# Kernel tuning notes

Measured on AMD Instinct MI355X. Metric: run time of the kernel, lower is better.

## Reference

```python
import jax, jax.numpy as jnp
import numpy as np

N, F, E, G = 50000, 128, 1600000, 64
CH = [16, 32, 64, 128, 256]
K = 3
EPS = 1e-5


def setup_inputs() -> dict:
    key = jax.random.key(0)
    ks = jax.random.split(key, 16)
    inp = {}
    inp["x"] = jax.random.normal(ks[0], (N, F), jnp.float32)
    inp["edge_weight"] = jax.random.uniform(ks[1], (E,), jnp.float32)
    inp["edge_index"] = jax.random.randint(ks[2], (2, E), 0, N)
    inp["batch_index"] = jnp.sort(jax.random.randint(ks[3], (N,), 0, G))
    dims = [F] + CH
    i = 4
    for l in range(5):
        fi, fo = dims[l], dims[l + 1]
        inp[f"W{l+1}"] = jax.random.normal(ks[i], (K, fi, fo), jnp.float32) / np.sqrt(K * fi)
        i += 1
        inp[f"b{l+1}"] = jnp.zeros((fo,), jnp.float32)
        if l < 4:  # no BN after the 5th conv
            inp[f"g{l+1}"] = jnp.ones((fo,), jnp.float32)
            inp[f"be{l+1}"] = jnp.zeros((fo,), jnp.float32)
    inp["Wd"] = jax.random.normal(ks[i], (2 * CH[-1], 4), jnp.float32) / np.sqrt(2 * CH[-1])
    inp["bd"] = jnp.zeros((4,), jnp.float32)
    inp["num_graphs"] = G
    return inp


def _bn(h, g, b):
    m = jnp.mean(h, axis=0)
    v = jnp.mean(jnp.square(h - m), axis=0)  # biased variance (torch training mode)
    return g * (h - m) / jnp.sqrt(v + EPS) + b


def reference(x, edge_weight, W1, b1, g1, be1, W2, b2, g2, be2, W3, b3, g3, be3,
              W4, b4, g4, be4, W5, b5, Wd, bd, edge_index, batch_index, num_graphs):
    n = x.shape[0]
    row, col = edge_index[0], edge_index[1]
    # sym-normalized Laplacian, lambda_max=2 -> scaled L_hat has zero diagonal,
    # off-diagonal = -w * deg^-1/2[row] * deg^-1/2[col]
    deg = jax.ops.segment_sum(edge_weight, row, num_segments=n)
    dinv = jnp.where(deg > 0, jax.lax.rsqrt(jnp.where(deg > 0, deg, 1.0)), 0.0)
    norm = -edge_weight * dinv[row] * dinv[col]

    def prop(z):  # L_hat @ z via sparse gather/scatter over edges
        return jax.ops.segment_sum(norm[:, None] * z[col], row, num_segments=n)

    def cheb(z, W, b):  # T0=z, T1=L z, T2=2 L T1 - T0
        t1 = prop(z)
        out = z @ W[0] + t1 @ W[1]
        t2 = 2.0 * prop(t1) - z
        return out + t2 @ W[2] + b

    h = _bn(jax.nn.softplus(cheb(x, W1, b1)), g1, be1)
    h = _bn(jax.nn.softplus(cheb(h, W2, b2)), g2, be2)
    h = _bn(jax.nn.softplus(cheb(h, W3, b3)), g3, be3)
    h = _bn(jax.nn.softplus(cheb(h, W4, b4)), g4, be4)
    h = cheb(h, W5, b5)

    mx = jax.ops.segment_max(h, batch_index, num_segments=num_graphs)
    mx = jnp.where(jnp.isfinite(mx), mx, 0.0)  # guard empty segments
    cnt = jax.ops.segment_sum(jnp.ones((n,), h.dtype), batch_index, num_segments=num_graphs)
    mean = jax.ops.segment_sum(h, batch_index, num_segments=num_graphs) / jnp.maximum(cnt, 1.0)[:, None]
    pooled = jnp.concatenate([mx, mean], axis=1)  # [G, 512]
    logits = pooled @ Wd + bd
    return jax.nn.log_softmax(logits, axis=-1)
```

## Files before the change

### kernel.cpp

```cpp
#include <hip/hip_runtime.h>
#include <hip/hip_fp16.h>
#include <cmath>

#define NN 50000
#define NE 1600000
#define NG 64
#define CAP 96
#define NPART 8
#define PROWS 6250

typedef __attribute__((ext_vector_type(8))) short short8_t;
typedef __attribute__((ext_vector_type(4))) float floatx4;
typedef __attribute__((ext_vector_type(4))) unsigned short us4;
typedef __attribute__((ext_vector_type(8))) unsigned short us8;

static __device__ __forceinline__ float softplusf(float x) {
    return fmaxf(x, 0.0f) + log1pf(expf(-fabsf(x)));
}

static __device__ __forceinline__ float bf2f(unsigned short u) {
    return __uint_as_float(((unsigned)u) << 16);
}
static __device__ __forceinline__ unsigned short f2bf(float x) {
    unsigned u = __float_as_uint(x);
    unsigned t = (u >> 16) & 1u;
    return (unsigned short)((u + 0x7FFFu + t) >> 16);
}
static __device__ __forceinline__ float h2f(unsigned u) {
    __half_raw r; r.x = (unsigned short)(u & 0xFFFFu);
    return __half2float(__half(r));
}
static __device__ __forceinline__ unsigned short f2h(float x) {
    __half h = __float2half_rn(x);
    return static_cast<__half_raw>(h).x;
}

static __device__ __forceinline__ void split_bf16(float x, unsigned short& hi, unsigned short& lo) {
    unsigned u = __float_as_uint(x);
    unsigned hb = u & 0xFFFF0000u;
    hi = (unsigned short)(hb >> 16);
    float r = x - __uint_as_float(hb);
    lo = f2bf(r);
}

__global__ __launch_bounds__(256) void k_slot2(const int* __restrict__ row,
                                               const int* __restrict__ col,
                                               const float* __restrict__ w,
                                               int* __restrict__ cnt,
                                               unsigned* __restrict__ pslots) {
    const int part = blockIdx.x & (NPART - 1);
    const int bid = blockIdx.x >> 3;
    const int nb = gridDim.x >> 3;
    const int rlo = part * PROWS;
    const int rhi = rlo + PROWS;
    for (int e = bid * 256 + threadIdx.x; e < NE; e += nb * 256) {
        int r = row[e];
        if (r >= rlo && r < rhi) {
            int k = atomicAdd(&cnt[r], 1);
            k = min(k, CAP - 1);
            pslots[(size_t)r * CAP + k] = ((unsigned)col[e] << 16) | (unsigned)f2h(w[e]);
        }
    }
}

__global__ __launch_bounds__(256) void k_degsum(const int* __restrict__ cnt,
                                                const unsigned* __restrict__ pslots,
                                                float* __restrict__ dinv) {
    int tid = threadIdx.x;
    int lane = tid & 15;
    int node = blockIdx.x * 16 + (tid >> 4);
    if (node >= NN) return;
    int e = cnt[node];
    const unsigned* base = pslots + (size_t)node * CAP;
    float s = 0.0f;
    for (int k = lane; k < e; k += 16) s += h2f(base[k]);
#pragma unroll
    for (int m = 8; m >= 1; m >>= 1) s += __shfl_xor(s, m);
    if (lane == 0) dinv[node] = (s > 0.0f) ? rsqrtf(s) : 0.0f;
}

__global__ __launch_bounds__(256) void k_repack(const int* __restrict__ cnt,
                                                unsigned* __restrict__ pslots,
                                                const float* __restrict__ dinv) {
    int tid = threadIdx.x;
    int lane = tid & 15;
    int node = blockIdx.x * 16 + (tid >> 4);
    if (node >= NN) return;
    int e = cnt[node];
    float dr = dinv[node];
    unsigned* pb = pslots + (size_t)node * CAP;
    for (int k = lane; k < e; k += 16) {
        unsigned s = pb[k];
        float wv = -h2f(s) * dr * dinv[s >> 16];
        pb[k] = (s & 0xFFFF0000u) | (unsigned)f2h(wv);
    }
}

__global__ void k_wcat1(const float* __restrict__ W1, float* __restrict__ wc) {
    int i = blockIdx.x * blockDim.x + threadIdx.x;
    if (i < 128 * 48) {
        int k = i / 48, j = i - k * 48;
        float v;
        if (j < 16)      v = W1[k * 16 + j] - W1[2 * 2048 + k * 16 + j];
        else if (j < 32) v = W1[2048 + k * 16 + (j - 16)];
        else             v = W1[2 * 2048 + k * 16 + (j - 32)];
        wc[i] = v;
    }
}

__global__ void k_wsplit(const float* __restrict__ W, int K, int N,
                         unsigned short* __restrict__ hiT, unsigned short* __restrict__ loT) {
    int idx = blockIdx.x * 256 + threadIdx.x;
    if (idx < K * N) {
        int k = idx / N, n = idx - k * N;
        unsigned short h, l;
        split_bf16(W[idx], h, l);
        hiT[(size_t)n * K + k] = h;
        loT[(size_t)n * K + k] = l;
    }
}

#define ASTR 40

__global__ __launch_bounds__(256, 2) void k_gemm_mfma_f32A(
    const float* __restrict__ A, int lda,
    const unsigned short* __restrict__ BhiT,
    const unsigned short* __restrict__ BloT,
    unsigned short* __restrict__ C, int ldc,
    int M, int K, int Ncol)
{
    __shared__ unsigned short Ah[128 * ASTR];
    __shared__ unsigned short Al[128 * ASTR];
    __shared__ unsigned short Bh[128 * ASTR];
    __shared__ unsigned short Bl[128 * ASTR];

    const int tid = threadIdx.x;
    const int lane = tid & 63;
    const int wave = tid >> 6;
    const int wm = wave >> 1, wn = wave & 1;
    const int quad = lane >> 4, l16 = lane & 15;
    const int bm = blockIdx.y * 128, bn = blockIdx.x * 128;
    const int srow = tid >> 1;
    const int skq  = (tid & 1) * 16;

    floatx4 acc[4][4];
#pragma unroll
    for (int i = 0; i < 4; ++i)
#pragma unroll
        for (int j = 0; j < 4; ++j) acc[i][j] = (floatx4){0.f, 0.f, 0.f, 0.f};

    for (int k0 = 0; k0 < K; k0 += 32) {
        float4 a0 = make_float4(0, 0, 0, 0), a1 = a0, a2 = a0, a3 = a0;
        const int ga = bm + srow;
        if (ga < M) {
            const float* Ap = A + (size_t)ga * lda + k0 + skq;
            a0 = *(const float4*)(Ap + 0);
            a1 = *(const float4*)(Ap + 4);
            a2 = *(const float4*)(Ap + 8);
            a3 = *(const float4*)(Ap + 12);
        }
        uint4 bh0 = make_uint4(0, 0, 0, 0), bh1 = bh0, bl0 = bh0, bl1 = bh0;
        const int gb = bn + srow;
        if (gb < Ncol) {
            const unsigned short* ph = BhiT + (size_t)gb * K + k0 + skq;
            const unsigned short* pl = BloT + (size_t)gb * K + k0 + skq;
            bh0 = *(const uint4*)(ph);
            bh1 = *(const uint4*)(ph + 8);
            bl0 = *(const uint4*)(pl);
            bl1 = *(const uint4*)(pl + 8);
        }
        __attribute__((aligned(16))) unsigned short ah[16], al[16];
        const float av[16] = {a0.x, a0.y, a0.z, a0.w, a1.x, a1.y, a1.z, a1.w,
                              a2.x, a2.y, a2.z, a2.w, a3.x, a3.y, a3.z, a3.w};
#pragma unroll
        for (int i = 0; i < 16; ++i) split_bf16(av[i], ah[i], al[i]);

        __syncthreads();
        *(uint4*)&Ah[srow * ASTR + skq]     = *(const uint4*)&ah[0];
        *(uint4*)&Ah[srow * ASTR + skq + 8] = *(const uint4*)&ah[8];
        *(uint4*)&Al[srow * ASTR + skq]     = *(const uint4*)&al[0];
        *(uint4*)&Al[srow * ASTR + skq + 8] = *(const uint4*)&al[8];
        *(uint4*)&Bh[srow * ASTR + skq]     = bh0;
        *(uint4*)&Bh[srow * ASTR + skq + 8] = bh1;
        *(uint4*)&Bl[srow * ASTR + skq]     = bl0;
        *(uint4*)&Bl[srow * ASTR + skq + 8] = bl1;
        __syncthreads();

        short8_t afh[4], afl[4], bfh[4], bfl[4];
#pragma unroll
        for (int t = 0; t < 4; ++t) {
            const int m = wm * 64 + t * 16 + l16;
            afh[t] = *(const short8_t*)&Ah[m * ASTR + quad * 8];
            afl[t] = *(const short8_t*)&Al[m * ASTR + quad * 8];
            const int n = wn * 64 + t * 16 + l16;
            bfh[t] = *(const short8_t*)&Bh[n * ASTR + quad * 8];
            bfl[t] = *(const short8_t*)&Bl[n * ASTR + quad * 8];
        }
#pragma unroll
        for (int i = 0; i < 4; ++i)
#pragma unroll
            for (int j = 0; j < 4; ++j) {
                acc[i][j] = __builtin_amdgcn_mfma_f32_16x16x32_bf16(afh[i], bfh[j], acc[i][j], 0, 0, 0);
                acc[i][j] = __builtin_amdgcn_mfma_f32_16x16x32_bf16(afh[i], bfl[j], acc[i][j], 0, 0, 0);
                acc[i][j] = __builtin_amdgcn_mfma_f32_16x16x32_bf16(afl[i], bfh[j], acc[i][j], 0, 0, 0);
            }
    }

#pragma unroll
    for (int j = 0; j < 4; ++j) {
        const int col = bn + wn * 64 + j * 16 + l16;
        if (col >= Ncol) continue;
#pragma unroll
        for (int i = 0; i < 4; ++i) {
#pragma unroll
            for (int r = 0; r < 4; ++r) {
                const int row = bm + wm * 64 + i * 16 + quad * 4 + r;
                if (row >= M) continue;
                C[(size_t)row * ldc + col] = f2bf(acc[i][j][r]);
            }
        }
    }
}

__global__ __launch_bounds__(256, 2) void k_gemm_mfma_bf(
    const unsigned short* __restrict__ A, int lda,
    const unsigned short* __restrict__ BhiT,
    const unsigned short* __restrict__ BloT,
    unsigned short* __restrict__ C, int ldc,
    int M, int K, int Ncol,
    const float* __restrict__ bias, int act)
{
    __shared__ unsigned short Ah[128 * ASTR];
    __shared__ unsigned short Bh[128 * ASTR];
    __shared__ unsigned short Bl[128 * ASTR];

    const int tid = threadIdx.x;
    const int lane = tid & 63;
    const int wave = tid >> 6;
    const int wm = wave >> 1, wn = wave & 1;
    const int quad = lane >> 4, l16 = lane & 15;
    const int bm = blockIdx.y * 128, bn = blockIdx.x * 128;
    const int srow = tid >> 1;
    const int skq  = (tid & 1) * 16;

    floatx4 acc[4][4];
#pragma unroll
    for (int i = 0; i < 4; ++i)
#pragma unroll
        for (int j = 0; j < 4; ++j) acc[i][j] = (floatx4){0.f, 0.f, 0.f, 0.f};

    for (int k0 = 0; k0 < K; k0 += 32) {
        uint4 a0 = make_uint4(0, 0, 0, 0), a1 = a0;
        const int ga = bm + srow;
        if (ga < M) {
            const unsigned short* Ap = A + (size_t)ga * lda + k0 + skq;
            a0 = *(const uint4*)(Ap);
            a1 = *(const uint4*)(Ap + 8);
        }
        uint4 bh0 = make_uint4(0, 0, 0, 0), bh1 = bh0, bl0 = bh0, bl1 = bh0;
        const int gb = bn + srow;
        if (gb < Ncol) {
            const unsigned short* ph = BhiT + (size_t)gb * K + k0 + skq;
            const unsigned short* pl = BloT + (size_t)gb * K + k0 + skq;
            bh0 = *(const uint4*)(ph);
            bh1 = *(const uint4*)(ph + 8);
            bl0 = *(const uint4*)(pl);
            bl1 = *(const uint4*)(pl + 8);
        }
        __syncthreads();
        *(uint4*)&Ah[srow * ASTR + skq]     = a0;
        *(uint4*)&Ah[srow * ASTR + skq + 8] = a1;
        *(uint4*)&Bh[srow * ASTR + skq]     = bh0;
        *(uint4*)&Bh[srow * ASTR + skq + 8] = bh1;
        *(uint4*)&Bl[srow * ASTR + skq]     = bl0;
        *(uint4*)&Bl[srow * ASTR + skq + 8] = bl1;
        __syncthreads();

        short8_t afh[4], bfh[4], bfl[4];
#pragma unroll
        for (int t = 0; t < 4; ++t) {
            const int m = wm * 64 + t * 16 + l16;
            afh[t] = *(const short8_t*)&Ah[m * ASTR + quad * 8];
            const int n = wn * 64 + t * 16 + l16;
            bfh[t] = *(const short8_t*)&Bh[n * ASTR + quad * 8];
            bfl[t] = *(const short8_t*)&Bl[n * ASTR + quad * 8];
        }
#pragma unroll
        for (int i = 0; i < 4; ++i)
#pragma unroll
            for (int j = 0; j < 4; ++j) {
                acc[i][j] = __builtin_amdgcn_mfma_f32_16x16x32_bf16(afh[i], bfh[j], acc[i][j], 0, 0, 0);
                acc[i][j] = __builtin_amdgcn_mfma_f32_16x16x32_bf16(afh[i], bfl[j], acc[i][j], 0, 0, 0);
            }
    }

#pragma unroll
    for (int j = 0; j < 4; ++j) {
        const int col = bn + wn * 64 + j * 16 + l16;
        if (col >= Ncol) continue;
        const float bv = bias ? bias[col] : 0.0f;
#pragma unroll
        for (int i = 0; i < 4; ++i) {
#pragma unroll
            for (int r = 0; r < 4; ++r) {
                const int row = bm + wm * 64 + i * 16 + quad * 4 + r;
                if (row >= M) continue;
                float v = acc[i][j][r] + bv;
                if (act) v = softplusf(v);
                C[(size_t)row * ldc + col] = f2bf(v);
            }
        }
    }
}

__global__ __launch_bounds__(256) void k_gemm(
    const unsigned short* __restrict__ A, int lda,
    const float* __restrict__ B, int ldb,
    unsigned short* __restrict__ C, int ldc,
    int M, int K, int Ncol,
    const float* __restrict__ bias, int act)
{
    __shared__ float As[16][128];
    __shared__ float Bs[16][128];
    const int tid = threadIdx.x;
    const int tx = tid & 15;
    const int ty = tid >> 4;
    const int bm = blockIdx.y * 128;
    const int bn = blockIdx.x * 128;
    const int arow = tid >> 1;
    const int akq = (tid & 1) * 8;
    const int bkr = tid >> 4;
    const int bcq = (tid & 15) * 8;

    float acc[8][8];
#pragma unroll
    for (int i = 0; i < 8; ++i)
#pragma unroll
        for (int j = 0; j < 8; ++j) acc[i][j] = 0.0f;

    for (int k0 = 0; k0 < K; k0 += 16) {
        uint4 ald = make_uint4(0, 0, 0, 0);
        int gr = bm + arow;
        if (gr < M) ald = *(const uint4*)(A + (size_t)gr * lda + k0 + akq);
        float4 b0 = make_float4(0, 0, 0, 0), b1 = make_float4(0, 0, 0, 0);
        int cb = bn + bcq;
        const float* Bp = B + (k0 + bkr) * ldb;
        if (cb < Ncol)     b0 = *(const float4*)(Bp + cb);
        if (cb + 4 < Ncol) b1 = *(const float4*)(Bp + cb + 4);
        __syncthreads();
        const unsigned short* au = (const unsigned short*)&ald;
#pragma unroll
        for (int i = 0; i < 8; ++i) As[akq + i][arow] = bf2f(au[i]);
        *(float4*)&Bs[bkr][bcq] = b0;
        *(float4*)&Bs[bkr][bcq + 4] = b1;
        __syncthreads();
#pragma unroll
        for (int kk = 0; kk < 16; ++kk) {
            float a[8], b[8];
            float4 t;
            t = *(const float4*)&As[kk][ty * 4];      a[0] = t.x; a[1] = t.y; a[2] = t.z; a[3] = t.w;
            t = *(const float4*)&As[kk][64 + ty * 4]; a[4] = t.x; a[5] = t.y; a[6] = t.z; a[7] = t.w;
            t = *(const float4*)&Bs[kk][tx * 4];      b[0] = t.x; b[1] = t.y; b[2] = t.z; b[3] = t.w;
            t = *(const float4*)&Bs[kk][64 + tx * 4]; b[4] = t.x; b[5] = t.y; b[6] = t.z; b[7] = t.w;
#pragma unroll
            for (int i = 0; i < 8; ++i)
#pragma unroll
                for (int j = 0; j < 8; ++j)
                    acc[i][j] = fmaf(a[i], b[j], acc[i][j]);
        }
    }
#pragma unroll
    for (int i = 0; i < 8; ++i) {
        int r = bm + ((i < 4) ? (ty * 4 + i) : (64 + ty * 4 + i - 4));
        if (r >= M) continue;
#pragma unroll
        for (int j = 0; j < 8; ++j) {
            int cl = bn + ((j < 4) ? (tx * 4 + j) : (64 + tx * 4 + j - 4));
            if (cl >= Ncol) continue;
            float v = acc[i][j];
            if (bias) v += bias[cl];
            if (act) v = softplusf(v);
            C[(size_t)r * ldc + cl] = f2bf(v);
        }
    }
}

__global__ __launch_bounds__(256) void k_prop(
    const int* __restrict__ cnt, const unsigned* __restrict__ pslots,
    const unsigned short* __restrict__ z, int zld, int zoff,
    unsigned short* __restrict__ out, int outld, int ooff,
    int ltw, float alpha,
    const unsigned short* __restrict__ add1, int a1ld, int a1off, float c1,
    const unsigned short* __restrict__ add2, int a2ld, int a2off,
    const float* __restrict__ bias, int act)
{
    const int T = 1 << ltw;
    const int lane = threadIdx.x & (T - 1);
    const int node = blockIdx.x * (256 >> ltw) + (threadIdx.x >> ltw);
    if (node >= NN) return;
    const int f4 = lane * 4;
    const int e = cnt[node];
    const unsigned* base = pslots + (size_t)node * CAP;
    float accA[4] = {0, 0, 0, 0};
    float accB[4] = {0, 0, 0, 0};
    const unsigned short* zp = z + zoff + f4;
    int p = 0;
    for (; p + 8 <= e; p += 8) {
        unsigned s0 = base[p + 0], s1 = base[p + 1], s2 = base[p + 2], s3 = base[p + 3];
        unsigned s4 = base[p + 4], s5 = base[p + 5], s6 = base[p + 6], s7 = base[p + 7];
        const us4 z0 = *(const us4*)(zp + (size_t)(s0 >> 16) * zld);
        const us4 z1 = *(const us4*)(zp + (size_t)(s1 >> 16) * zld);
        const us4 z2 = *(const us4*)(zp + (size_t)(s2 >> 16) * zld);
        const us4 z3 = *(const us4*)(zp + (size_t)(s3 >> 16) * zld);
        const us4 z4 = *(const us4*)(zp + (size_t)(s4 >> 16) * zld);
        const us4 z5 = *(const us4*)(zp + (size_t)(s5 >> 16) * zld);
        const us4 z6 = *(const us4*)(zp + (size_t)(s6 >> 16) * zld);
        const us4 z7 = *(const us4*)(zp + (size_t)(s7 >> 16) * zld);
        float w0 = h2f(s0), w1 = h2f(s1), w2 = h2f(s2), w3 = h2f(s3);
        float w4 = h2f(s4), w5 = h2f(s5), w6 = h2f(s6), w7 = h2f(s7);
#pragma unroll
        for (int i = 0; i < 4; ++i) {
            accA[i] = fmaf(w0, bf2f(z0[i]), accA[i]);
            accB[i] = fmaf(w1, bf2f(z1[i]), accB[i]);
            accA[i] = fmaf(w2, bf2f(z2[i]), accA[i]);
            accB[i] = fmaf(w3, bf2f(z3[i]), accB[i]);
            accA[i] = fmaf(w4, bf2f(z4[i]), accA[i]);
            accB[i] = fmaf(w5, bf2f(z5[i]), accB[i]);
            accA[i] = fmaf(w6, bf2f(z6[i]), accA[i]);
            accB[i] = fmaf(w7, bf2f(z7[i]), accB[i]);
        }
    }
    for (; p + 4 <= e; p += 4) {
        unsigned s0 = base[p + 0], s1 = base[p + 1], s2 = base[p + 2], s3 = base[p + 3];
        const us4 z0 = *(const us4*)(zp + (size_t)(s0 >> 16) * zld);
        const us4 z1 = *(const us4*)(zp + (size_t)(s1 >> 16) * zld);
        const us4 z2 = *(const us4*)(zp + (size_t)(s2 >> 16) * zld);
        const us4 z3 = *(const us4*)(zp + (size_t)(s3 >> 16) * zld);
        float w0 = h2f(s0), w1 = h2f(s1), w2 = h2f(s2), w3 = h2f(s3);
#pragma unroll
        for (int i = 0; i < 4; ++i) {
            accA[i] = fmaf(w0, bf2f(z0[i]), accA[i]);
            accB[i] = fmaf(w1, bf2f(z1[i]), accB[i]);
            accA[i] = fmaf(w2, bf2f(z2[i]), accA[i]);
            accB[i] = fmaf(w3, bf2f(z3[i]), accB[i]);
        }
    }
    for (; p < e; ++p) {
        unsigned s = base[p];
        float wv = h2f(s);
        const us4 zv = *(const us4*)(zp + (size_t)(s >> 16) * zld);
#pragma unroll
        for (int i = 0; i < 4; ++i) accA[i] = fmaf(wv, bf2f(zv[i]), accA[i]);
    }
#pragma unroll
    for (int i = 0; i < 4; ++i) accA[i] = alpha * (accA[i] + accB[i]);
    if (add1) {
        const us4 t = *(const us4*)(add1 + (size_t)node * a1ld + a1off + f4);
#pragma unroll
        for (int i = 0; i < 4; ++i) accA[i] = fmaf(c1, bf2f(t[i]), accA[i]);
    }
    if (add2) {
        const us4 t = *(const us4*)(add2 + (size_t)node * a2ld + a2off + f4);
#pragma unroll
        for (int i = 0; i < 4; ++i) accA[i] += bf2f(t[i]);
    }
    if (bias) {
        const float4 t = *(const float4*)(bias + f4);
        accA[0] += t.x; accA[1] += t.y; accA[2] += t.z; accA[3] += t.w;
    }
    if (act) {
#pragma unroll
        for (int i = 0; i < 4; ++i) accA[i] = softplusf(accA[i]);
    }
    us4 o;
#pragma unroll
    for (int i = 0; i < 4; ++i) o[i] = f2bf(accA[i]);
    *(us4*)(out + (size_t)node * outld + ooff + f4) = o;
}

__global__ __launch_bounds__(256) void k_bnstats(const unsigned short* __restrict__ h, int ld, int lc,
                                                 float* __restrict__ stats) {
    const int C = 1 << lc;
    const int tid = threadIdx.x;
    const int c = tid & (C - 1);
    const int rpb = 256 >> lc;
    int r = blockIdx.x * rpb + (tid >> lc);
    const int stride = gridDim.x * rpb;
    float s = 0.0f, q = 0.0f;
    for (; r < NN; r += stride) {
        float v = bf2f(h[(size_t)r * ld + c]);
        s += v;
        q = fmaf(v, v, q);
    }
    __shared__ float shs[256], shq[256];
    shs[tid] = s; shq[tid] = q;
    __syncthreads();
    for (int o = 128; o >= C; o >>= 1) {
        if (tid < o) { shs[tid] += shs[tid + o]; shq[tid] += shq[tid + o]; }
        __syncthreads();
    }
    if (tid < C) {
        atomicAdd(&stats[c], shs[tid]);
        atomicAdd(&stats[128 + c], shq[tid]);
    }
}

__global__ void k_bnapply(unsigned short* __restrict__ h, int ld, int lc,
                          const float* __restrict__ stats,
                          const float* __restrict__ g, const float* __restrict__ be) {
    int idx = blockIdx.x * 256 + threadIdx.x;
    const int C8 = 1 << (lc - 3);
    if (idx >= NN * C8) return;
    int r = idx >> (lc - 3);
    int c0 = (idx & (C8 - 1)) << 3;
    const float invN = 1.0f / (float)NN;
    unsigned short* hp = h + (size_t)r * ld + c0;
    us8 v = *(const us8*)hp;
    us8 o;
#pragma unroll
    for (int i = 0; i < 8; ++i) {
        int c = c0 + i;
        float m = stats[c] * invN;
        float var = fmaf(stats[128 + c], invN, -m * m);
        var = fmaxf(var, 0.0f);
        float inv = rsqrtf(var + 1e-5f);
        o[i] = f2bf(fmaf(g[c] * inv, bf2f(v[i]) - m, be[c]));
    }
    *(us8*)hp = o;
}

static __device__ __forceinline__ int lower_bound_dev(const int* __restrict__ b, int val) {
    int lo = 0, hi = NN;
    while (lo < hi) {
        int mid = (lo + hi) >> 1;
        if (b[mid] < val) lo = mid + 1; else hi = mid;
    }
    return lo;
}

__global__ void k_gbounds(const int* __restrict__ batch, int* __restrict__ gb) {
    int g = threadIdx.x;
    if (g <= NG) gb[g] = (g == NG) ? NN : lower_bound_dev(batch, g);
}

__global__ __launch_bounds__(256) void k_pool1(const unsigned short* __restrict__ h,
                                               const int* __restrict__ gb,
                                               float* __restrict__ partial) {
    int g = blockIdx.y;
    int j = blockIdx.x;
    int start = gb[g], end = gb[g + 1];
    int len = end - start;
    int chunk = (len + 15) >> 4;
    int s = start + j * chunk;
    int e = min(s + chunk, end);
    int c = threadIdx.x;
    float mx = -INFINITY, sum = 0.0f;
    for (int r = s; r < e; ++r) {
        float v = bf2f(h[(size_t)r * 256 + c]);
        mx = fmaxf(mx, v);
        sum += v;
    }
    size_t base = ((size_t)(g * 16 + j)) * 512;
    partial[base + c] = mx;
    partial[base + 256 + c] = sum;
}

__global__ __launch_bounds__(256) void k_pool2d(const float* __restrict__ partial,
                                                const int* __restrict__ gb,
                                                const float* __restrict__ Wd,
                                                const float* __restrict__ bd,
                                                float* __restrict__ out) {
    __shared__ float pl[512];
    __shared__ float red[4][256];
    int g = blockIdx.x;
    int c = threadIdx.x;
    float mx = -INFINITY, sum = 0.0f;
#pragma unroll
    for (int j = 0; j < 16; ++j) {
        size_t base = ((size_t)(g * 16 + j)) * 512;
        mx = fmaxf(mx, partial[base + c]);
        sum += partial[base + 256 + c];
    }
    int len = gb[g + 1] - gb[g];
    pl[c] = (len > 0) ? mx : 0.0f;
    pl[256 + c] = sum / fmaxf((float)len, 1.0f);
    __syncthreads();
    float p[4] = {0, 0, 0, 0};
    for (int k = c; k < 512; k += 256) {
        float pv = pl[k];
#pragma unroll
        for (int cc = 0; cc < 4; ++cc) p[cc] = fmaf(pv, Wd[k * 4 + cc], p[cc]);
    }
#pragma unroll
    for (int cc = 0; cc < 4; ++cc) red[cc][c] = p[cc];
    __syncthreads();
    for (int o = 128; o >= 1; o >>= 1) {
        if (c < o) {
#pragma unroll
            for (int cc = 0; cc < 4; ++cc) red[cc][c] += red[cc][c + o];
        }
        __syncthreads();
    }
    if (c == 0) {
        float l0 = red[0][0] + bd[0], l1 = red[1][0] + bd[1];
        float l2 = red[2][0] + bd[2], l3 = red[3][0] + bd[3];
        float m = fmaxf(fmaxf(l0, l1), fmaxf(l2, l3));
        float ls = m + logf(expf(l0 - m) + expf(l1 - m) + expf(l2 - m) + expf(l3 - m));
        out[g * 4 + 0] = l0 - ls;
        out[g * 4 + 1] = l1 - ls;
        out[g * 4 + 2] = l2 - ls;
        out[g * 4 + 3] = l3 - ls;
    }
}

extern "C" void kernel_launch(void* const* d_in, const int* in_sizes, int n_in,
                              void* d_out, int out_size, void* d_ws, size_t ws_size,
                              hipStream_t stream)
{
    const float* x    = (const float*)d_in[0];
    const float* ew   = (const float*)d_in[1];
    const int*   row  = (const int*)d_in[2];
    const int*   colp = row + NE;
    const int*   batch = (const int*)d_in[3];
    const float* W1 = (const float*)d_in[4];
    const float* b1 = (const float*)d_in[5];
    const float* g1 = (const float*)d_in[6];
    const float* be1 = (const float*)d_in[7];
    const float* W2 = (const float*)d_in[8];
    const float* b2 = (const float*)d_in[9];
    const float* g2 = (const float*)d_in[10];
    const float* be2 = (const float*)d_in[11];
    const float* W3 = (const float*)d_in[12];
    const float* b3 = (const float*)d_in[13];
    const float* g3 = (const float*)d_in[14];
    const float* be3 = (const float*)d_in[15];
    const float* W4 = (const float*)d_in[16];
    const float* b4 = (const float*)d_in[17];
    const float* g4 = (const float*)d_in[18];
    const float* be4 = (const float*)d_in[19];
    const float* W5 = (const float*)d_in[20];
    const float* b5 = (const float*)d_in[21];
    const float* Wd = (const float*)d_in[22];
    const float* bd = (const float*)d_in[23];
    float* outp = (float*)d_out;
    (void)in_sizes; (void)n_in; (void)out_size; (void)ws_size; (void)ew;

    char* wsb = (char*)d_ws;
    size_t off = 0;
    auto take = [&](size_t bytes) -> void* {
        void* p = wsb + off;
        off = (off + bytes + 255) & ~(size_t)255;
        return p;
    };
    int*   cnt    = (int*)take((size_t)NN * sizeof(int));
    float* dinv   = (float*)take((size_t)NN * sizeof(float));
    int*   gb     = (int*)take((NG + 1) * sizeof(int));
    unsigned* pslots = (unsigned*)take((size_t)NN * CAP * sizeof(unsigned));
    float* statsA = (float*)take(4 * 256 * sizeof(float));
    float* wcat   = (float*)take(6144 * sizeof(float));
    unsigned short* bt1h = (unsigned short*)take(48 * 128 * 2);
    unsigned short* bt1l = (unsigned short*)take(48 * 128 * 2);
    unsigned short* bt3h = (unsigned short*)take(64 * 96 * 2);
    unsigned short* bt3l = (unsigned short*)take(64 * 96 * 2);
    unsigned short* bt4h = (unsigned short*)take(128 * 192 * 2);
    unsigned short* bt4l = (unsigned short*)take(128 * 192 * 2);
    unsigned short* bt5h = (unsigned short*)take(256 * 384 * 2);
    unsigned short* bt5l = (unsigned short*)take(256 * 384 * 2);
    float* partial= (float*)take((size_t)NG * 16 * 512 * sizeof(float));
    unsigned short* P   = (unsigned short*)take((size_t)NN * 48 * 2);
    unsigned short* uv  = (unsigned short*)take((size_t)NN * 32 * 2);
    unsigned short* Hc2 = (unsigned short*)take((size_t)NN * 48 * 2);
    unsigned short* Hc3 = (unsigned short*)take((size_t)NN * 96 * 2);
    unsigned short* Hc4 = (unsigned short*)take((size_t)NN * 192 * 2);
    unsigned short* Hc5 = (unsigned short*)take((size_t)NN * 384 * 2);
    unsigned short* h5  = (unsigned short*)take((size_t)NN * 256 * 2);

    float* stats1 = statsA;
    float* stats2 = statsA + 256;
    float* stats3 = statsA + 512;
    float* stats4 = statsA + 768;

    hipMemsetAsync(cnt, 0, NN * sizeof(int), stream);
    hipMemsetAsync(statsA, 0, 4 * 256 * sizeof(float), stream);

    k_slot2<<<2048, 256, 0, stream>>>(row, colp, ew, cnt, pslots);
    k_degsum<<<3125, 256, 0, stream>>>(cnt, pslots, dinv);
    k_repack<<<3125, 256, 0, stream>>>(cnt, pslots, dinv);

    k_wcat1<<<24, 256, 0, stream>>>(W1, wcat);
    k_gbounds<<<1, 128, 0, stream>>>(batch, gb);
    k_wsplit<<<24, 256, 0, stream>>>(wcat, 128, 48, bt1h, bt1l);
    k_wsplit<<<24, 256, 0, stream>>>(W3, 96, 64, bt3h, bt3l);
    k_wsplit<<<96, 256, 0, stream>>>(W4, 192, 128, bt4h, bt4l);
    k_wsplit<<<384, 256, 0, stream>>>(W5, 384, 256, bt5h, bt5l);

    k_gemm_mfma_f32A<<<dim3(1, 391), 256, 0, stream>>>(x, 128, bt1h, bt1l, P, 48, NN, 128, 48);
    k_prop<<<1563, 256, 0, stream>>>(cnt, pslots, P, 48, 16, uv, 32, 0, 3, 1.0f,
                                     nullptr, 0, 0, 0.0f, nullptr, 0, 0, nullptr, 0);
    k_prop<<<782, 256, 0, stream>>>(cnt, pslots, uv, 32, 16, Hc2, 48, 0, 2, 2.0f,
                                    P, 48, 0, 1.0f, uv, 32, 0, b1, 1);
    k_bnstats<<<256, 256, 0, stream>>>(Hc2, 48, 4, stats1);
    k_bnapply<<<391, 256, 0, stream>>>(Hc2, 48, 4, stats1, g1, be1);

    k_prop<<<782, 256, 0, stream>>>(cnt, pslots, Hc2, 48, 0, Hc2, 48, 16, 2, 1.0f,
                                    nullptr, 0, 0, 0.0f, nullptr, 0, 0, nullptr, 0);
    k_prop<<<782, 256, 0, stream>>>(cnt, pslots, Hc2, 48, 16, Hc2, 48, 32, 2, 2.0f,
                                    Hc2, 48, 0, -1.0f, nullptr, 0, 0, nullptr, 0);
    k_gemm<<<dim3(1, 391), 256, 0, stream>>>(Hc2, 48, W2, 32, Hc3, 96, NN, 48, 32, b2, 1);
    k_bnstats<<<256, 256, 0, stream>>>(Hc3, 96, 5, stats2);
    k_bnapply<<<782, 256, 0, stream>>>(Hc3, 96, 5, stats2, g2, be2);

    k_prop<<<1563, 256, 0, stream>>>(cnt, pslots, Hc3, 96, 0, Hc3, 96, 32, 3, 1.0f,
                                     nullptr, 0, 0, 0.0f, nullptr, 0, 0, nullptr, 0);
    k_prop<<<1563, 256, 0, stream>>>(cnt, pslots, Hc3, 96, 32, Hc3, 96, 64, 3, 2.0f,
                                     Hc3, 96, 0, -1.0f, nullptr, 0, 0, nullptr, 0);
    k_gemm_mfma_bf<<<dim3(1, 391), 256, 0, stream>>>(Hc3, 96, bt3h, bt3l, Hc4, 192, NN, 96, 64, b3, 1);
    k_bnstats<<<256, 256, 0, stream>>>(Hc4, 192, 6, stats3);
    k_bnapply<<<1563, 256, 0, stream>>>(Hc4, 192, 6, stats3, g3, be3);

    k_prop<<<3125, 256, 0, stream>>>(cnt, pslots, Hc4, 192, 0, Hc4, 192, 64, 4, 1.0f,
                                     nullptr, 0, 0, 0.0f, nullptr, 0, 0, nullptr, 0);
    k_prop<<<3125, 256, 0, stream>>>(cnt, pslots, Hc4, 192, 64, Hc4, 192, 128, 4, 2.0f,
                                     Hc4, 192, 0, -1.0f, nullptr, 0, 0, nullptr, 0);
    k_gemm_mfma_bf<<<dim3(1, 391), 256, 0, stream>>>(Hc4, 192, bt4h, bt4l, Hc5, 384, NN, 192, 128, b4, 1);
    k_bnstats<<<256, 256, 0, stream>>>(Hc5, 384, 7, stats4);
    k_bnapply<<<3125, 256, 0, stream>>>(Hc5, 384, 7, stats4, g4, be4);

    k_prop<<<6250, 256, 0, stream>>>(cnt, pslots, Hc5, 384, 0, Hc5, 384, 128, 5, 1.0f,
                                     nullptr, 0, 0, 0.0f, nullptr, 0, 0, nullptr, 0);
    k_prop<<<6250, 256, 0, stream>>>(cnt, pslots, Hc5, 384, 128, Hc5, 384, 256, 5, 2.0f,
                                     Hc5, 384, 0, -1.0f, nullptr, 0, 0, nullptr, 0);
    k_gemm_mfma_bf<<<dim3(2, 391), 256, 0, stream>>>(Hc5, 384, bt5h, bt5l, h5, 256, NN, 384, 256, b5, 0);

    k_pool1<<<dim3(16, 64), 256, 0, stream>>>(h5, gb, partial);
    k_pool2d<<<64, 256, 0, stream>>>(partial, gb, Wd, bd, outp);
}
```

Before: 799.0 us.

## Merge weight prep kernels and co-schedule edge slotting with first GEMM

Six small setup launches (wcat, gbounds, four wsplits) are folded into one k_prep kernel that also writes the W1 combination directly in split bf16 form. The edge slot-building scatter and the first-layer GEMM are fused into one heterogeneous launch, with every sixth block doing a GEMM tile, so the compute-bound GEMM overlaps the atomic-bound scatter. The aim is to cut launch overhead and idle gaps between kernels. In exchange the fused kernel carries GEMM shared memory and launch bounds into the scatter blocks, which may lower their occupancy.

```diff
diff --git a/kernel.cpp b/kernel.cpp
--- a/kernel.cpp
+++ b/kernel.cpp
@@ -43,22 +43,200 @@
     lo = f2bf(r);
 }
 
-__global__ __launch_bounds__(256) void k_slot2(const int* __restrict__ row,
-                                               const int* __restrict__ col,
-                                               const float* __restrict__ w,
-                                               int* __restrict__ cnt,
-                                               unsigned* __restrict__ pslots) {
-    const int part = blockIdx.x & (NPART - 1);
-    const int bid = blockIdx.x >> 3;
-    const int nb = gridDim.x >> 3;
-    const int rlo = part * PROWS;
-    const int rhi = rlo + PROWS;
-    for (int e = bid * 256 + threadIdx.x; e < NE; e += nb * 256) {
-        int r = row[e];
-        if (r >= rlo && r < rhi) {
-            int k = atomicAdd(&cnt[r], 1);
-            k = min(k, CAP - 1);
-            pslots[(size_t)r * CAP + k] = ((unsigned)col[e] << 16) | (unsigned)f2h(w[e]);
+static __device__ __forceinline__ int lower_bound_dev(const int* __restrict__ b, int val) {
+    int lo = 0, hi = NN;
+    while (lo < hi) {
+        int mid = (lo + hi) >> 1;
+        if (b[mid] < val) lo = mid + 1; else hi = mid;
+    }
+    return lo;
+}
+
+__global__ __launch_bounds__(256) void k_prep(
+    const float* __restrict__ W1, const float* __restrict__ W3,
+    const float* __restrict__ W4, const float* __restrict__ W5,
+    const int* __restrict__ batch,
+    unsigned short* __restrict__ bt1h, unsigned short* __restrict__ bt1l,
+    unsigned short* __restrict__ bt3h, unsigned short* __restrict__ bt3l,
+    unsigned short* __restrict__ bt4h, unsigned short* __restrict__ bt4l,
+    unsigned short* __restrict__ bt5h, unsigned short* __restrict__ bt5l,
+    int* __restrict__ gb)
+{
+    const int bx = blockIdx.x;
+    const int tid = threadIdx.x;
+    if (bx < 24) {
+        int idx = bx * 256 + tid;
+        if (idx < 128 * 48) {
+            int k = idx / 48, j = idx - k * 48;
+            float v;
+            if (j < 16)      v = W1[k * 16 + j] - W1[2 * 2048 + k * 16 + j];
+            else if (j < 32) v = W1[2048 + k * 16 + (j - 16)];
+            else             v = W1[2 * 2048 + k * 16 + (j - 32)];
+            unsigned short h, l;
+            split_bf16(v, h, l);
+            bt1h[(size_t)j * 128 + k] = h;
+            bt1l[(size_t)j * 128 + k] = l;
+        }
+    } else if (bx < 48) {
+        int idx = (bx - 24) * 256 + tid;
+        if (idx < 96 * 64) {
+            int k = idx / 64, n = idx - k * 64;
+            unsigned short h, l;
+            split_bf16(W3[idx], h, l);
+            bt3h[(size_t)n * 96 + k] = h;
+            bt3l[(size_t)n * 96 + k] = l;
+        }
+    } else if (bx < 144) {
+        int idx = (bx - 48) * 256 + tid;
+        if (idx < 192 * 128) {
+            int k = idx / 128, n = idx - k * 128;
+            unsigned short h, l;
+            split_bf16(W4[idx], h, l);
+            bt4h[(size_t)n * 192 + k] = h;
+            bt4l[(size_t)n * 192 + k] = l;
+        }
+    } else if (bx < 528) {
+        int idx = (bx - 144) * 256 + tid;
+        if (idx < 384 * 256) {
+            int k = idx / 256, n = idx - k * 256;
+            unsigned short h, l;
+            split_bf16(W5[idx], h, l);
+            bt5h[(size_t)n * 384 + k] = h;
+            bt5l[(size_t)n * 384 + k] = l;
+        }
+    } else {
+        int g = tid;
+        if (g <= NG) gb[g] = (g == NG) ? NN : lower_bound_dev(batch, g);
+    }
+}
+
+#define ASTR 40
+
+__global__ __launch_bounds__(256, 2) void k_build1(
+    const int* __restrict__ row, const int* __restrict__ col,
+    const float* __restrict__ w,
+    int* __restrict__ cnt, unsigned* __restrict__ pslots,
+    const float* __restrict__ A,
+    const unsigned short* __restrict__ BhiT,
+    const unsigned short* __restrict__ BloT,
+    unsigned short* __restrict__ C)
+{
+    __shared__ unsigned short Ah[128 * ASTR];
+    __shared__ unsigned short Al[128 * ASTR];
+    __shared__ unsigned short Bh[128 * ASTR];
+    __shared__ unsigned short Bl[128 * ASTR];
+
+    const unsigned bx = blockIdx.x;
+    const int tid = threadIdx.x;
+    int gemmT = -1, sid = 0;
+    if (bx < 2346u) {
+        if (bx % 6u == 5u) gemmT = bx / 6u;
+        else sid = bx - (bx + 1u) / 6u;
+    } else {
+        sid = bx - 391u;
+    }
+
+    if (gemmT < 0) {
+        const int part = sid & (NPART - 1);
+        const int bid = sid >> 3;
+        const int nb = 2048 >> 3;
+        const int rlo = part * PROWS;
+        const int rhi = rlo + PROWS;
+        for (int e = bid * 256 + tid; e < NE; e += nb * 256) {
+            int r = row[e];
+            if (r >= rlo && r < rhi) {
+                int k = atomicAdd(&cnt[r], 1);
+                k = min(k, CAP - 1);
+                pslots[(size_t)r * CAP + k] = ((unsigned)col[e] << 16) | (unsigned)f2h(w[e]);
+            }
+        }
+        return;
+    }
+
+    const int lda = 128, ldc = 48, M = NN, K = 128, Ncol = 48;
+    const int lane = tid & 63;
+    const int wave = tid >> 6;
+    const int wm = wave >> 1, wn = wave & 1;
+    const int quad = lane >> 4, l16 = lane & 15;
+    const int bm = gemmT * 128, bn = 0;
+    const int srow = tid >> 1;
+    const int skq  = (tid & 1) * 16;
+
+    floatx4 acc[4][4];
+#pragma unroll
+    for (int i = 0; i < 4; ++i)
+#pragma unroll
+        for (int j = 0; j < 4; ++j) acc[i][j] = (floatx4){0.f, 0.f, 0.f, 0.f};
+
+    for (int k0 = 0; k0 < K; k0 += 32) {
+        float4 a0 = make_float4(0, 0, 0, 0), a1 = a0, a2 = a0, a3 = a0;
+        const int ga = bm + srow;
+        if (ga < M) {
+            const float* Ap = A + (size_t)ga * lda + k0 + skq;
+            a0 = *(const float4*)(Ap + 0);
+            a1 = *(const float4*)(Ap + 4);
+            a2 = *(const float4*)(Ap + 8);
+            a3 = *(const float4*)(Ap + 12);
+        }
+        uint4 bh0 = make_uint4(0, 0, 0, 0), bh1 = bh0, bl0 = bh0, bl1 = bh0;
+        const int gb2 = bn + srow;
+        if (gb2 < Ncol) {
+            const unsigned short* ph = BhiT + (size_t)gb2 * K + k0 + skq;
+            const unsigned short* pl = BloT + (size_t)gb2 * K + k0 + skq;
+            bh0 = *(const uint4*)(ph);
+            bh1 = *(const uint4*)(ph + 8);
+            bl0 = *(const uint4*)(pl);
+            bl1 = *(const uint4*)(pl + 8);
+        }
+        __attribute__((aligned(16))) unsigned short ah[16], al[16];
+        const float av[16] = {a0.x, a0.y, a0.z, a0.w, a1.x, a1.y, a1.z, a1.w,
+                              a2.x, a2.y, a2.z, a2.w, a3.x, a3.y, a3.z, a3.w};
+#pragma unroll
+        for (int i = 0; i < 16; ++i) split_bf16(av[i], ah[i], al[i]);
+
+        __syncthreads();
+        *(uint4*)&Ah[srow * ASTR + skq]     = *(const uint4*)&ah[0];
+        *(uint4*)&Ah[srow * ASTR + skq + 8] = *(const uint4*)&ah[8];
+        *(uint4*)&Al[srow * ASTR + skq]     = *(const uint4*)&al[0];
+        *(uint4*)&Al[srow * ASTR + skq + 8] = *(const uint4*)&al[8];
+        *(uint4*)&Bh[srow * ASTR + skq]     = bh0;
+        *(uint4*)&Bh[srow * ASTR + skq + 8] = bh1;
+        *(uint4*)&Bl[srow * ASTR + skq]     = bl0;
+        *(uint4*)&Bl[srow * ASTR + skq + 8] = bl1;
+        __syncthreads();
+
+        short8_t afh[4], afl[4], bfh[4], bfl[4];
+#pragma unroll
+        for (int t = 0; t < 4; ++t) {
+            const int m = wm * 64 + t * 16 + l16;
+            afh[t] = *(const short8_t*)&Ah[m * ASTR + quad * 8];
+            afl[t] = *(const short8_t*)&Al[m * ASTR + quad * 8];
+            const int n = wn * 64 + t * 16 + l16;
+            bfh[t] = *(const short8_t*)&Bh[n * ASTR + quad * 8];
+            bfl[t] = *(const short8_t*)&Bl[n * ASTR + quad * 8];
+        }
+#pragma unroll
+        for (int i = 0; i < 4; ++i)
+#pragma unroll
+            for (int j = 0; j < 4; ++j) {
+                acc[i][j] = __builtin_amdgcn_mfma_f32_16x16x32_bf16(afh[i], bfh[j], acc[i][j], 0, 0, 0);
+                acc[i][j] = __builtin_amdgcn_mfma_f32_16x16x32_bf16(afh[i], bfl[j], acc[i][j], 0, 0, 0);
+                acc[i][j] = __builtin_amdgcn_mfma_f32_16x16x32_bf16(afl[i], bfh[j], acc[i][j], 0, 0, 0);
+            }
+    }
+
+#pragma unroll
+    for (int j = 0; j < 4; ++j) {
+        const int colc = bn + wn * 64 + j * 16 + l16;
+        if (colc >= Ncol) continue;
+#pragma unroll
+        for (int i = 0; i < 4; ++i) {
+#pragma unroll
+            for (int r = 0; r < 4; ++r) {
+                const int rowc = bm + wm * 64 + i * 16 + quad * 4 + r;
+                if (rowc >= M) continue;
+                C[(size_t)rowc * ldc + colc] = f2bf(acc[i][j][r]);
+            }
         }
     }
 }
@@ -93,132 +271,6 @@
         unsigned s = pb[k];
         float wv = -h2f(s) * dr * dinv[s >> 16];
         pb[k] = (s & 0xFFFF0000u) | (unsigned)f2h(wv);
-    }
-}
-
-__global__ void k_wcat1(const float* __restrict__ W1, float* __restrict__ wc) {
-    int i = blockIdx.x * blockDim.x + threadIdx.x;
-    if (i < 128 * 48) {
-        int k = i / 48, j = i - k * 48;
-        float v;
-        if (j < 16)      v = W1[k * 16 + j] - W1[2 * 2048 + k * 16 + j];
-        else if (j < 32) v = W1[2048 + k * 16 + (j - 16)];
-        else             v = W1[2 * 2048 + k * 16 + (j - 32)];
-        wc[i] = v;
-    }
-}
-
-__global__ void k_wsplit(const float* __restrict__ W, int K, int N,
-                         unsigned short* __restrict__ hiT, unsigned short* __restrict__ loT) {
-    int idx = blockIdx.x * 256 + threadIdx.x;
-    if (idx < K * N) {
-        int k = idx / N, n = idx - k * N;
-        unsigned short h, l;
-        split_bf16(W[idx], h, l);
-        hiT[(size_t)n * K + k] = h;
-        loT[(size_t)n * K + k] = l;
-    }
-}
-
-#define ASTR 40
-
-__global__ __launch_bounds__(256, 2) void k_gemm_mfma_f32A(
-    const float* __restrict__ A, int lda,
-    const unsigned short* __restrict__ BhiT,
-    const unsigned short* __restrict__ BloT,
-    unsigned short* __restrict__ C, int ldc,
-    int M, int K, int Ncol)
-{
-    __shared__ unsigned short Ah[128 * ASTR];
-    __shared__ unsigned short Al[128 * ASTR];
-    __shared__ unsigned short Bh[128 * ASTR];
-    __shared__ unsigned short Bl[128 * ASTR];
-
-    const int tid = threadIdx.x;
-    const int lane = tid & 63;
-    const int wave = tid >> 6;
-    const int wm = wave >> 1, wn = wave & 1;
-    const int quad = lane >> 4, l16 = lane & 15;
-    const int bm = blockIdx.y * 128, bn = blockIdx.x * 128;
-    const int srow = tid >> 1;
-    const int skq  = (tid & 1) * 16;
-
-    floatx4 acc[4][4];
-#pragma unroll
-    for (int i = 0; i < 4; ++i)
-#pragma unroll
-        for (int j = 0; j < 4; ++j) acc[i][j] = (floatx4){0.f, 0.f, 0.f, 0.f};
-
-    for (int k0 = 0; k0 < K; k0 += 32) {
-        float4 a0 = make_float4(0, 0, 0, 0), a1 = a0, a2 = a0, a3 = a0;
-        const int ga = bm + srow;
-        if (ga < M) {
-            const float* Ap = A + (size_t)ga * lda + k0 + skq;
-            a0 = *(const float4*)(Ap + 0);
-            a1 = *(const float4*)(Ap + 4);
-            a2 = *(const float4*)(Ap + 8);
-            a3 = *(const float4*)(Ap + 12);
-        }
-        uint4 bh0 = make_uint4(0, 0, 0, 0), bh1 = bh0, bl0 = bh0, bl1 = bh0;
-        const int gb = bn + srow;
-        if (gb < Ncol) {
-            const unsigned short* ph = BhiT + (size_t)gb * K + k0 + skq;
-            const unsigned short* pl = BloT + (size_t)gb * K + k0 + skq;
-            bh0 = *(const uint4*)(ph);
-            bh1 = *(const uint4*)(ph + 8);
-            bl0 = *(const uint4*)(pl);
-            bl1 = *(const uint4*)(pl + 8);
-        }
-        __attribute__((aligned(16))) unsigned short ah[16], al[16];
-        const float av[16] = {a0.x, a0.y, a0.z, a0.w, a1.x, a1.y, a1.z, a1.w,
-                              a2.x, a2.y, a2.z, a2.w, a3.x, a3.y, a3.z, a3.w};
-#pragma unroll
-        for (int i = 0; i < 16; ++i) split_bf16(av[i], ah[i], al[i]);
-
-        __syncthreads();
-        *(uint4*)&Ah[srow * ASTR + skq]     = *(const uint4*)&ah[0];
-        *(uint4*)&Ah[srow * ASTR + skq + 8] = *(const uint4*)&ah[8];
-        *(uint4*)&Al[srow * ASTR + skq]     = *(const uint4*)&al[0];
-        *(uint4*)&Al[srow * ASTR + skq + 8] = *(const uint4*)&al[8];
-        *(uint4*)&Bh[srow * ASTR + skq]     = bh0;
-        *(uint4*)&Bh[srow * ASTR + skq + 8] = bh1;
-        *(uint4*)&Bl[srow * ASTR + skq]     = bl0;
-        *(uint4*)&Bl[srow * ASTR + skq + 8] = bl1;
-        __syncthreads();
-
-        short8_t afh[4], afl[4], bfh[4], bfl[4];
-#pragma unroll
-        for (int t = 0; t < 4; ++t) {
-            const int m = wm * 64 + t * 16 + l16;
-            afh[t] = *(const short8_t*)&Ah[m * ASTR + quad * 8];
-            afl[t] = *(const short8_t*)&Al[m * ASTR + quad * 8];
-            const int n = wn * 64 + t * 16 + l16;
-            bfh[t] = *(const short8_t*)&Bh[n * ASTR + quad * 8];
-            bfl[t] = *(const short8_t*)&Bl[n * ASTR + quad * 8];
-        }
-#pragma unroll
-        for (int i = 0; i < 4; ++i)
-#pragma unroll
-            for (int j = 0; j < 4; ++j) {
-                acc[i][j] = __builtin_amdgcn_mfma_f32_16x16x32_bf16(afh[i], bfh[j], acc[i][j], 0, 0, 0);
-                acc[i][j] = __builtin_amdgcn_mfma_f32_16x16x32_bf16(afh[i], bfl[j], acc[i][j], 0, 0, 0);
-                acc[i][j] = __builtin_amdgcn_mfma_f32_16x16x32_bf16(afl[i], bfh[j], acc[i][j], 0, 0, 0);
-            }
-    }
-
-#pragma unroll
-    for (int j = 0; j < 4; ++j) {
-        const int col = bn + wn * 64 + j * 16 + l16;
-        if (col >= Ncol) continue;
-#pragma unroll
-        for (int i = 0; i < 4; ++i) {
-#pragma unroll
-            for (int r = 0; r < 4; ++r) {
-                const int row = bm + wm * 64 + i * 16 + quad * 4 + r;
-                if (row >= M) continue;
-                C[(size_t)row * ldc + col] = f2bf(acc[i][j][r]);
-            }
-        }
     }
 }
 
@@ -529,20 +581,6 @@
     *(us8*)hp = o;
 }
 
-static __device__ __forceinline__ int lower_bound_dev(const int* __restrict__ b, int val) {
-    int lo = 0, hi = NN;
-    while (lo < hi) {
-        int mid = (lo + hi) >> 1;
-        if (b[mid] < val) lo = mid + 1; else hi = mid;
-    }
-    return lo;
-}
-
-__global__ void k_gbounds(const int* __restrict__ batch, int* __restrict__ gb) {
-    int g = threadIdx.x;
-    if (g <= NG) gb[g] = (g == NG) ? NN : lower_bound_dev(batch, g);
-}
-
 __global__ __launch_bounds__(256) void k_pool1(const unsigned short* __restrict__ h,
                                                const int* __restrict__ gb,
                                                float* __restrict__ partial) {
@@ -674,6 +712,7 @@
     unsigned short* Hc4 = (unsigned short*)take((size_t)NN * 192 * 2);
     unsigned short* Hc5 = (unsigned short*)take((size_t)NN * 384 * 2);
     unsigned short* h5  = (unsigned short*)take((size_t)NN * 256 * 2);
+    (void)wcat;
 
     float* stats1 = statsA;
     float* stats2 = statsA + 256;
@@ -683,18 +722,15 @@
     hipMemsetAsync(cnt, 0, NN * sizeof(int), stream);
     hipMemsetAsync(statsA, 0, 4 * 256 * sizeof(float), stream);
 
-    k_slot2<<<2048, 256, 0, stream>>>(row, colp, ew, cnt, pslots);
+    k_prep<<<529, 256, 0, stream>>>(W1, W3, W4, W5, batch,
+                                    bt1h, bt1l, bt3h, bt3l, bt4h, bt4l,
+                                    bt5h, bt5l, gb);
+
+    k_build1<<<2439, 256, 0, stream>>>(row, colp, ew, cnt, pslots,
+                                       x, bt1h, bt1l, P);
     k_degsum<<<3125, 256, 0, stream>>>(cnt, pslots, dinv);
     k_repack<<<3125, 256, 0, stream>>>(cnt, pslots, dinv);
 
-    k_wcat1<<<24, 256, 0, stream>>>(W1, wcat);
-    k_gbounds<<<1, 128, 0, stream>>>(batch, gb);
-    k_wsplit<<<24, 256, 0, stream>>>(wcat, 128, 48, bt1h, bt1l);
-    k_wsplit<<<24, 256, 0, stream>>>(W3, 96, 64, bt3h, bt3l);
-    k_wsplit<<<96, 256, 0, stream>>>(W4, 192, 128, bt4h, bt4l);
-    k_wsplit<<<384, 256, 0, stream>>>(W5, 384, 256, bt5h, bt5l);
-
-    k_gemm_mfma_f32A<<<dim3(1, 391), 256, 0, stream>>>(x, 128, bt1h, bt1l, P, 48, NN, 128, 48);
     k_prop<<<1563, 256, 0, stream>>>(cnt, pslots, P, 48, 16, uv, 32, 0, 3, 1.0f,
                                      nullptr, 0, 0, 0.0f, nullptr, 0, 0, nullptr, 0);
     k_prop<<<782, 256, 0, stream>>>(cnt, pslots, uv, 32, 16, Hc2, 48, 0, 2, 2.0f,
```

Result: no change. 795.5 us (-0.4%).
